# Kernel tuning notes

Measured on AMD Instinct MI355X. Metric: run time of the kernel, lower is better.

Reference implementation:

```python
import jax, jax.numpy as jnp
import numpy as np

NUM_THINGS = 80
NUM_STUFF = 53
IGNORE_CLASS = NUM_THINGS + NUM_STUFF  # 133, default ignore_class == -1 path
OVERLAP_THR = 0.5
STUFF_AREA_THR = 4096
THING_CONF_THR = 0.5
INSTANCE_OFFSET = 1000
NUM_SEM_CLASSES = NUM_THINGS + NUM_STUFF + 1  # label range [0, 133]


def setup_inputs() -> dict:
    key = jax.random.key(0)
    k1, k2, k3, k4 = jax.random.split(key, 4)
    B, N, H, W = 2, 100, 800, 1344
    ins_masks = jax.random.randint(k1, (B, N, H, W), 0, 2).astype(jnp.bool_)
    ins_scores = jax.random.uniform(k2, (B, N), dtype=jnp.float32)
    ins_class_ids = jax.random.randint(k3, (B, N), 0, NUM_THINGS, dtype=jnp.int32)
    sem_masks = jax.random.randint(k4, (B, H, W), 0, NUM_SEM_CLASSES, dtype=jnp.int32)
    return {"ins_masks": ins_masks, "ins_scores": ins_scores,
            "ins_class_ids": ins_class_ids, "sem_masks": sem_masks}


def _combine_segms(masks, scores, cls_ids, sem):
    # masks: [N,H,W] bool, scores: [N] f32, cls_ids: [N] i32, sem: [H,W] i32
    order = jnp.argsort(-scores)  # descending by score
    masks = masks[order]
    scores = scores[order]
    cls_ids = cls_ids[order]

    def step(carry, xs):
        pan, iid = carry  # pan: [H,W] i32, iid: i32 (next instance id)
        m, s, c = xs
        area = jnp.sum(m).astype(jnp.float32)
        inter = jnp.sum(m & (pan != 0)).astype(jnp.float32)
        keep = (s >= THING_CONF_THR) & (area > 0) & (inter <= OVERLAP_THR * area)
        write = keep & m & (pan == 0)  # only overwrite free pixels
        pan = jnp.where(write, c + iid * INSTANCE_OFFSET, pan)
        iid = iid + keep.astype(jnp.int32)
        return (pan, iid), None

    pan0 = jnp.zeros(masks.shape[1:], dtype=jnp.int32)
    (pan, _), _ = jax.lax.scan(step, (pan0, jnp.int32(1)), (masks, scores, cls_ids))

    # Stuff fusion: pixels claimed by things become ignore class, then any
    # remaining semantic class with area >= thr (and not ignored) is written.
    sem2 = jnp.where(pan > 0, IGNORE_CLASS, sem)
    counts = jnp.zeros((NUM_SEM_CLASSES,), jnp.int32).at[sem2.ravel()].add(1)
    valid = counts >= STUFF_AREA_THR
    valid = valid.at[IGNORE_CLASS].set(False)
    pan = jnp.where(valid[sem2], sem2 + NUM_THINGS, pan)
    return pan


def reference(ins_masks, ins_scores, ins_class_ids, sem_masks):
    # Batched greedy panoptic fusion -> [B,H,W] int32
    return jax.vmap(_combine_segms)(ins_masks, ins_scores, ins_class_ids, sem_masks)
```

## Files before the change

### kernel.cpp

```cpp
#include <hip/hip_runtime.h>
#include <stdint.h>

#define NB 2
#define NN 100
#define HWP (800*1344)
#define GCH 10
#define NCHMAX 10
#define NKEY (1<<(GCH+1))
#define CBIT (1u<<GCH)
#define NSEM 134
#define IGN 133
#define THR 1024
#define BPI 128
#define GRID (NB*BPI)
#define PPB (HWP/BPI)
#define GPX 8
#define NG (PPB/GPX)

struct WS {
  unsigned hist[NCHMAX][NB][NKEY];
  unsigned counts[NB][NSEM];
  int      iid[NB][NN];
  int      order[NB][NN];
  float    score_s[NB][NN];
  int      cls_s[NB][NN];
  unsigned kcAfter[NCHMAX][NB];
  unsigned Mcnt[NB];
  unsigned flag;
};
#define ZW (NCHMAX*NB*NKEY + NB*NSEM + NB*NN)

__device__ __forceinline__ unsigned u8x8_to_bits(uint2 v) {
  unsigned lo = (((v.x & 0x01010101u) * 0x01020408u) >> 24) & 0xFu;
  unsigned hi = (((v.y & 0x01010101u) * 0x01020408u) >> 24) & 0xFu;
  return lo | (hi << 4);
}

__device__ __forceinline__ unsigned load8(const void* __restrict__ masks,
                                          size_t eo, int mode_u8) {
  if (mode_u8) return u8x8_to_bits(*(const uint2*)((const uint8_t*)masks + eo));
  const uint4* mp = (const uint4*)((const int*)masks + eo);
  uint4 a = mp[0], b = mp[1];
  return (a.x & 1u) | ((a.y & 1u) << 1) | ((a.z & 1u) << 2) | ((a.w & 1u) << 3) |
         ((b.x & 1u) << 4) | ((b.y & 1u) << 5) | ((b.z & 1u) << 6) | ((b.w & 1u) << 7);
}

__global__ __launch_bounds__(THR) void k0_setup(
    const void* __restrict__ masks, const float* __restrict__ scores,
    const int* __restrict__ cls, WS* __restrict__ ws, uint8_t* __restrict__ owner) {
  const int t = threadIdx.x, gid = blockIdx.x;
  unsigned tg = (unsigned)gid * THR + t;
  if (tg < (unsigned)ZW) (&ws->hist[0][0][0])[tg] = 0;
  uint4* ow = (uint4*)owner;
  const unsigned nw = (unsigned)(NB * HWP / 16);
  for (unsigned i = tg; i < nw; i += (unsigned)GRID * THR)
    ow[i] = make_uint4(~0u, ~0u, ~0u, ~0u);
  if (gid == 0) {
    __shared__ float ss[NB * NN];
    __shared__ unsigned shDet;
    const unsigned* mw = (const unsigned*)masks;
    unsigned any = 0;
    for (int i = t; i < 4096; i += THR) any |= (mw[i] > 1u) ? 1u : 0u;
    if (t == 0) shDet = 0;
    if (t < NB * NN) ss[t] = scores[t];
    if (t < NB) ws->Mcnt[t] = 0;
    __syncthreads();
    if (any) atomicOr(&shDet, 1u);
    __syncthreads();
    if (t == 0) ws->flag = shDet;
    if (t < NB * NN) {
      int bb = t / NN, i = t % NN;
      float s = ss[bb * NN + i];
      if (s >= 0.5f) {
        int r = 0;
        for (int j = 0; j < NN; ++j) {
          float sj = ss[bb * NN + j];
          if (sj >= 0.5f && (sj > s || (sj == s && j < i))) r++;
        }
        ws->order[bb][r]   = i;
        ws->score_s[bb][r] = s;
        ws->cls_s[bb][r]   = cls[bb * NN + i];
        atomicAdd(&ws->Mcnt[bb], 1u);
      }
    }
  }
}

__global__ __launch_bounds__(THR, 4) void k_chunk(
    const void* __restrict__ masks, const int* __restrict__ sem,
    WS* __restrict__ ws, uint8_t* __restrict__ owner,
    int c, int doHist, int doCounts) {
  __shared__ unsigned lh[NKEY];
  __shared__ int midx[GCH];
  __shared__ int pmidx[GCH];
  __shared__ unsigned sh_kmask;
  const int t = threadIdx.x, gid = blockIdx.x;
  const int b = gid / BPI, bx = gid % BPI;
  const int M = (int)ws->Mcnt[b];
  int Lp = (c > 0) ? (M - (c - 1) * GCH) : 0; if (Lp > GCH) Lp = GCH;
  int Lc = doHist ? (M - c * GCH) : 0;        if (Lc > GCH) Lc = GCH;
  if (!doCounts && Lp <= 0 && Lc <= 0) return;

  if (Lp > 0) {
    if (t < GCH) pmidx[t] = ws->order[b][(c - 1) * GCH + t];
    if (t < 64) {
      const unsigned* __restrict__ hp = &ws->hist[c - 1][b][0];
      unsigned h[32];
      #pragma unroll
      for (int j = 0; j < 32; ++j) h[j] = hp[t + (j << 6)];
      unsigned km = 0;
      unsigned kc = (c >= 2) ? ws->kcAfter[c - 2][b] : 0u;
      for (int g = 0; g < Lp; ++g) {
        unsigned sel = km & ((1u << g) - 1u);
        unsigned area = 0, inter = 0;
        #pragma unroll
        for (int j = 0; j < 32; ++j) {
          unsigned i = (unsigned)t + ((unsigned)j << 6);
          if ((i >> g) & 1u) {
            area += h[j];
            if ((i >> GCH) | (i & sel)) inter += h[j];
          }
        }
        #pragma unroll
        for (int off = 32; off; off >>= 1) {
          area  += __shfl_xor(area, off);
          inter += __shfl_xor(inter, off);
        }
        float s = ws->score_s[b][(c - 1) * GCH + g];
        bool keep = (s >= 0.5f) && (area > 0u) && (2u * inter <= area);
        if (keep) {
          km |= 1u << g; kc += 1u;
          if (t == 0 && bx == 0) ws->iid[b][(c - 1) * GCH + g] = (int)kc;
        }
      }
      if (t == 0) { sh_kmask = km; if (bx == 0) ws->kcAfter[c - 1][b] = kc; }
    }
  } else if (t == 0) sh_kmask = 0;

  if (Lc > 0) {
    for (int i = t; i < NKEY; i += THR) lh[i] = 0;
    if (t < GCH) midx[t] = ws->order[b][(t < Lc) ? (c * GCH + t) : (c * GCH)];
  } else if (doCounts) {
    for (int i = t; i < NSEM; i += THR) lh[i] = 0;
  }
  __syncthreads();

  const unsigned kmask = sh_kmask;
  const int mode_u8 = (int)ws->flag;
  const size_t sbase = (size_t)b * HWP + (size_t)bx * PPB;
  const unsigned lm = (Lc >= GCH) ? (CBIT - 1u) : ((Lc > 0) ? ((1u << Lc) - 1u) : 0u);
  int midx_r[GCH], pmidx_r[GCH];
  if (Lc > 0) {
    #pragma unroll
    for (int g = 0; g < GCH; ++g) midx_r[g] = __builtin_amdgcn_readfirstlane(midx[g]);
  }
  if (kmask) {
    #pragma unroll
    for (int g = 0; g < GCH; ++g) pmidx_r[g] = __builtin_amdgcn_readfirstlane(pmidx[g]);
  }

  for (int s = 0; s < 2; ++s) {
    int gr = s * THR + t;
    if (gr >= NG) break;
    const int l0 = gr * GPX;
    const size_t off = (size_t)bx * PPB + l0;
    unsigned w2[2];
    unsigned free8;
    if (c <= 1) {
      w2[0] = ~0u; w2[1] = ~0u; free8 = 0xFFu;
    } else {
      uint2 ov = *(const uint2*)(owner + sbase + l0);
      w2[0] = ov.x; w2[1] = ov.y;
      free8 = 0;
      #pragma unroll
      for (int k = 0; k < GPX; ++k)
        if (((w2[k >> 2] >> ((k & 3) * 8)) & 0xFFu) == 0xFFu) free8 |= 1u << k;
    }
    if (kmask) {
      unsigned rem = kmask;
      bool chg = false;
      while (rem && free8) {
        int g = __builtin_ctz(rem); rem &= rem - 1u;
        unsigned b8 = load8(masks, (size_t)(b * NN + pmidx_r[g]) * HWP + off, mode_u8);
        unsigned take = b8 & free8;
        if (take) {
          unsigned rank = (unsigned)((c - 1) * GCH + g);
          #pragma unroll
          for (int k = 0; k < GPX; ++k)
            if ((take >> k) & 1u)
              w2[k >> 2] = (w2[k >> 2] & ~(0xFFu << ((k & 3) * 8))) |
                           (rank << ((k & 3) * 8));
          free8 &= ~take; chg = true;
        }
      }
      if (chg) *(uint2*)(owner + sbase + l0) = make_uint2(w2[0], w2[1]);
    }
    const unsigned claimed8 = ~free8 & 0xFFu;

    if (Lc > 0) {
      unsigned key[GPX];
      #pragma unroll
      for (int k = 0; k < GPX; ++k)
        key[k] = ((claimed8 >> k) & 1u) << GCH;
      if (mode_u8) {
        #pragma unroll
        for (int g = 0; g < GCH; ++g) {
          unsigned b8 = u8x8_to_bits(*(const uint2*)((const uint8_t*)masks +
              (size_t)(b * NN + midx_r[g]) * HWP + off));
          #pragma unroll
          for (int k = 0; k < GPX; ++k) key[k] |= ((b8 >> k) & 1u) << g;
        }
      } else {
        #pragma unroll 2
        for (int g = 0; g < GCH; ++g) {
          unsigned b8 = load8(masks, (size_t)(b * NN + midx_r[g]) * HWP + off, 0);
          #pragma unroll
          for (int k = 0; k < GPX; ++k) key[k] |= ((b8 >> k) & 1u) << g;
        }
      }
      #pragma unroll
      for (int k = 0; k < GPX; ++k)
        atomicAdd(&lh[key[k] & (lm | CBIT)], 1u);
    }
    if (doCounts) {
      const uint4* sp = (const uint4*)(sem + sbase + l0);
      uint4 sv0 = sp[0], sv1 = sp[1];
      unsigned sarr[8] = {sv0.x, sv0.y, sv0.z, sv0.w, sv1.x, sv1.y, sv1.z, sv1.w};
      #pragma unroll
      for (int k = 0; k < GPX; ++k)
        if (((free8 >> k) & 1u) && sarr[k] != (unsigned)IGN)
          atomicAdd(&lh[sarr[k]], 1u);
    }
  }
  __syncthreads();
  if (Lc > 0) {
    for (int i = t; i < NKEY; i += THR) {
      unsigned v = lh[i];
      if (v) atomicAdd(&ws->hist[c][b][i], v);
    }
  } else if (doCounts) {
    for (int i = t; i < NSEM; i += THR) {
      unsigned v = lh[i];
      if (v) atomicAdd(&ws->counts[b][i], v);
    }
  }
}

__global__ __launch_bounds__(THR) void k_writepan(
    const int* __restrict__ sem, const uint8_t* __restrict__ owner,
    const WS* __restrict__ ws, int* __restrict__ out) {
  __shared__ int pval[NN];
  __shared__ int sval[NSEM];
  const int t = threadIdx.x, gid = blockIdx.x;
  const int b = gid / BPI, bx = gid % BPI;
  const size_t sbase = (size_t)b * HWP + (size_t)bx * PPB;
  if (t < NN)  pval[t] = ws->cls_s[b][t] + ws->iid[b][t] * 1000;
  if (t < NSEM) sval[t] = (t != IGN && ws->counts[b][t] >= 4096u) ? (t + 80) : 0;
  __syncthreads();
  for (int s = 0; s < 2; ++s) {
    int gr = s * THR + t;
    if (gr >= NG) break;
    int l0 = gr * GPX;
    uint2 ov = *(const uint2*)(owner + sbase + l0);
    unsigned w2[2] = {ov.x, ov.y};
    const uint4* sp = (const uint4*)(sem + sbase + l0);
    uint4 sv0 = sp[0], sv1 = sp[1];
    unsigned sarr[8] = {sv0.x, sv0.y, sv0.z, sv0.w, sv1.x, sv1.y, sv1.z, sv1.w};
    int4* op = (int4*)(out + sbase + l0);
    #pragma unroll
    for (int q = 0; q < 2; ++q) {
      int res[4];
      #pragma unroll
      for (int j = 0; j < 4; ++j) {
        int k = q * 4 + j;
        unsigned by = (w2[k >> 2] >> ((k & 3) * 8)) & 0xFFu;
        res[j] = (by != 0xFFu) ? pval[by] : sval[sarr[k]];
      }
      op[q] = make_int4(res[0], res[1], res[2], res[3]);
    }
  }
}

extern "C" void kernel_launch(void* const* d_in, const int* in_sizes, int n_in,
                              void* d_out, int out_size, void* d_ws, size_t ws_size,
                              hipStream_t stream) {
  const void*  masks  = d_in[0];
  const float* scores = (const float*)d_in[1];
  const int*   cls    = (const int*)d_in[2];
  const int*   sem    = (const int*)d_in[3];
  int* out = (int*)d_out;

  uint8_t* base = (uint8_t*)d_ws;
  WS* ws = (WS*)base;
  size_t off = (sizeof(WS) + 255) & ~(size_t)255;
  uint8_t* owner = base + off;

  hipLaunchKernelGGL(k0_setup, dim3(GRID), dim3(THR), 0, stream,
                     masks, scores, cls, ws, owner);
  for (int c = 0; c < NCHMAX; ++c)
    hipLaunchKernelGGL(k_chunk, dim3(GRID), dim3(THR), 0, stream,
                       masks, sem, ws, owner, c, 1, 0);
  hipLaunchKernelGGL(k_chunk, dim3(GRID), dim3(THR), 0, stream,
                     masks, sem, ws, owner, NCHMAX, 0, 1);
  hipLaunchKernelGGL(k_writepan, dim3(GRID), dim3(THR), 0, stream,
                     sem, owner, ws, out);
}
```

Before: 178.5 us.

## Resolve chunk keep decisions in last block and spread histogram atomics

The greedy keep/iid decision for each chunk now runs once, in the last block to finish (chosen by an atomic ticket), and is stored in global kmask and kcAfter arrays. Previously every block of the next launch recomputed it from the histogram. Global histogram accumulation is spread over 8 copies indexed by block to reduce atomic contention, and the last block sums them. This removes redundant per-block prologue work in exchange for a threadfence and ticket atomic per block, a larger workspace to zero, and fewer maximum chunks (NCHMAX 8).

```diff
diff --git a/kernel.cpp b/kernel.cpp
--- a/kernel.cpp
+++ b/kernel.cpp
@@ -5,7 +5,7 @@
 #define NN 100
 #define HWP (800*1344)
 #define GCH 10
-#define NCHMAX 10
+#define NCHMAX 8
 #define NKEY (1<<(GCH+1))
 #define CBIT (1u<<GCH)
 #define NSEM 134
@@ -16,19 +16,22 @@
 #define PPB (HWP/BPI)
 #define GPX 8
 #define NG (PPB/GPX)
+#define NCPY 8
 
 struct WS {
-  unsigned hist[NCHMAX][NB][NKEY];
+  unsigned hist8[NCPY][NCHMAX][NB][NKEY];
   unsigned counts[NB][NSEM];
   int      iid[NB][NN];
+  unsigned ticket[NCHMAX][NB];
+  unsigned kmaskArr[NCHMAX][NB];
+  unsigned kcAfter[NCHMAX][NB];
   int      order[NB][NN];
   float    score_s[NB][NN];
   int      cls_s[NB][NN];
-  unsigned kcAfter[NCHMAX][NB];
   unsigned Mcnt[NB];
   unsigned flag;
 };
-#define ZW (NCHMAX*NB*NKEY + NB*NSEM + NB*NN)
+#define ZW (NCPY*NCHMAX*NB*NKEY + NB*NSEM + NB*NN + NCHMAX*NB*3)
 
 __device__ __forceinline__ unsigned u8x8_to_bits(uint2 v) {
   unsigned lo = (((v.x & 0x01010101u) * 0x01020408u) >> 24) & 0xFu;
@@ -49,11 +52,12 @@
     const void* __restrict__ masks, const float* __restrict__ scores,
     const int* __restrict__ cls, WS* __restrict__ ws, uint8_t* __restrict__ owner) {
   const int t = threadIdx.x, gid = blockIdx.x;
-  unsigned tg = (unsigned)gid * THR + t;
-  if (tg < (unsigned)ZW) (&ws->hist[0][0][0])[tg] = 0;
+  unsigned* zp = &ws->hist8[0][0][0][0];
+  for (unsigned i = (unsigned)gid * THR + t; i < (unsigned)ZW; i += (unsigned)GRID * THR)
+    zp[i] = 0;
   uint4* ow = (uint4*)owner;
   const unsigned nw = (unsigned)(NB * HWP / 16);
-  for (unsigned i = tg; i < nw; i += (unsigned)GRID * THR)
+  for (unsigned i = (unsigned)gid * THR + t; i < nw; i += (unsigned)GRID * THR)
     ow[i] = make_uint4(~0u, ~0u, ~0u, ~0u);
   if (gid == 0) {
     __shared__ float ss[NB * NN];
@@ -93,7 +97,7 @@
   __shared__ unsigned lh[NKEY];
   __shared__ int midx[GCH];
   __shared__ int pmidx[GCH];
-  __shared__ unsigned sh_kmask;
+  __shared__ unsigned sh_tic;
   const int t = threadIdx.x, gid = blockIdx.x;
   const int b = gid / BPI, bx = gid % BPI;
   const int M = (int)ws->Mcnt[b];
@@ -101,54 +105,18 @@
   int Lc = doHist ? (M - c * GCH) : 0;        if (Lc > GCH) Lc = GCH;
   if (!doCounts && Lp <= 0 && Lc <= 0) return;
 
-  if (Lp > 0) {
-    if (t < GCH) pmidx[t] = ws->order[b][(c - 1) * GCH + t];
-    if (t < 64) {
-      const unsigned* __restrict__ hp = &ws->hist[c - 1][b][0];
-      unsigned h[32];
-      #pragma unroll
-      for (int j = 0; j < 32; ++j) h[j] = hp[t + (j << 6)];
-      unsigned km = 0;
-      unsigned kc = (c >= 2) ? ws->kcAfter[c - 2][b] : 0u;
-      for (int g = 0; g < Lp; ++g) {
-        unsigned sel = km & ((1u << g) - 1u);
-        unsigned area = 0, inter = 0;
-        #pragma unroll
-        for (int j = 0; j < 32; ++j) {
-          unsigned i = (unsigned)t + ((unsigned)j << 6);
-          if ((i >> g) & 1u) {
-            area += h[j];
-            if ((i >> GCH) | (i & sel)) inter += h[j];
-          }
-        }
-        #pragma unroll
-        for (int off = 32; off; off >>= 1) {
-          area  += __shfl_xor(area, off);
-          inter += __shfl_xor(inter, off);
-        }
-        float s = ws->score_s[b][(c - 1) * GCH + g];
-        bool keep = (s >= 0.5f) && (area > 0u) && (2u * inter <= area);
-        if (keep) {
-          km |= 1u << g; kc += 1u;
-          if (t == 0 && bx == 0) ws->iid[b][(c - 1) * GCH + g] = (int)kc;
-        }
-      }
-      if (t == 0) { sh_kmask = km; if (bx == 0) ws->kcAfter[c - 1][b] = kc; }
-    }
-  } else if (t == 0) sh_kmask = 0;
-
+  const unsigned kmask = (Lp > 0) ? ws->kmaskArr[c - 1][b] : 0u;
   if (Lc > 0) {
     for (int i = t; i < NKEY; i += THR) lh[i] = 0;
     if (t < GCH) midx[t] = ws->order[b][(t < Lc) ? (c * GCH + t) : (c * GCH)];
   } else if (doCounts) {
     for (int i = t; i < NSEM; i += THR) lh[i] = 0;
   }
+  if (kmask && t < GCH) pmidx[t] = ws->order[b][(c - 1) * GCH + t];
   __syncthreads();
 
-  const unsigned kmask = sh_kmask;
   const int mode_u8 = (int)ws->flag;
   const size_t sbase = (size_t)b * HWP + (size_t)bx * PPB;
-  const unsigned lm = (Lc >= GCH) ? (CBIT - 1u) : ((Lc > 0) ? ((1u << Lc) - 1u) : 0u);
   int midx_r[GCH], pmidx_r[GCH];
   if (Lc > 0) {
     #pragma unroll
@@ -219,8 +187,7 @@
         }
       }
       #pragma unroll
-      for (int k = 0; k < GPX; ++k)
-        atomicAdd(&lh[key[k] & (lm | CBIT)], 1u);
+      for (int k = 0; k < GPX; ++k) atomicAdd(&lh[key[k]], 1u);
     }
     if (doCounts) {
       const uint4* sp = (const uint4*)(sem + sbase + l0);
@@ -233,10 +200,58 @@
     }
   }
   __syncthreads();
+
   if (Lc > 0) {
+    unsigned* hp = &ws->hist8[bx & (NCPY - 1)][c][b][0];
     for (int i = t; i < NKEY; i += THR) {
       unsigned v = lh[i];
-      if (v) atomicAdd(&ws->hist[c][b][i], v);
+      if (v) atomicAdd(&hp[i], v);
+    }
+    __threadfence();
+    if (t == 0) sh_tic = atomicAdd(&ws->ticket[c][b], 1u);
+    __syncthreads();
+    if (sh_tic == (unsigned)(BPI - 1)) {
+      __threadfence();
+      for (int i = t; i < NKEY; i += THR) {
+        unsigned v = 0;
+        #pragma unroll
+        for (int s8 = 0; s8 < NCPY; ++s8)
+          v += __hip_atomic_load(&ws->hist8[s8][c][b][i],
+                                 __ATOMIC_RELAXED, __HIP_MEMORY_SCOPE_AGENT);
+        lh[i] = v;
+      }
+      __syncthreads();
+      if (t < 64) {
+        unsigned h[32];
+        #pragma unroll
+        for (int j = 0; j < 32; ++j) h[j] = lh[t + (j << 6)];
+        unsigned km = 0;
+        unsigned kc = (c >= 1) ? ws->kcAfter[c - 1][b] : 0u;
+        for (int g = 0; g < Lc; ++g) {
+          unsigned sel = km & ((1u << g) - 1u);
+          unsigned area = 0, inter = 0;
+          #pragma unroll
+          for (int j = 0; j < 32; ++j) {
+            unsigned i = (unsigned)t + ((unsigned)j << 6);
+            if ((i >> g) & 1u) {
+              area += h[j];
+              if ((i >> GCH) | (i & sel)) inter += h[j];
+            }
+          }
+          #pragma unroll
+          for (int off = 32; off; off >>= 1) {
+            area  += __shfl_xor(area, off);
+            inter += __shfl_xor(inter, off);
+          }
+          float s = ws->score_s[b][c * GCH + g];
+          bool keep = (s >= 0.5f) && (area > 0u) && (2u * inter <= area);
+          if (keep) {
+            km |= 1u << g; kc += 1u;
+            if (t == 0) ws->iid[b][c * GCH + g] = (int)kc;
+          }
+        }
+        if (t == 0) { ws->kmaskArr[c][b] = km; ws->kcAfter[c][b] = kc; }
+      }
     }
   } else if (doCounts) {
     for (int i = t; i < NSEM; i += THR) {
```

Measured after the change: 521.5 us. +192.2%, slower.
